# Kernel tuning notes

Hardware: AMD Instinct MI355X
Metric: run time of the kernel (lower is better)

## Reference

```python
import jax, jax.numpy as jnp
import numpy as np
from jax import lax

C, H, O = 95, 128, 4
B, T = 256, 1000
EPS = 1e-5


def setup_inputs() -> dict:
    key = jax.random.key(0)
    ks = jax.random.split(key, 8)
    x = jax.random.normal(ks[0], (B, T, C), dtype=jnp.float32)
    # BatchNorm1d params (eval mode: running stats)
    gamma = jnp.ones((C,), jnp.float32)
    beta = jnp.zeros((C,), jnp.float32)
    running_mean = jnp.zeros((C,), jnp.float32)
    running_var = jnp.ones((C,), jnp.float32)
    # LSTM params, torch gate order (i, f, g, o), init U(-1/sqrt(H), 1/sqrt(H))
    s = 1.0 / np.sqrt(H)
    W_ih = jax.random.uniform(ks[1], (4 * H, C), jnp.float32, -s, s)
    W_hh = jax.random.uniform(ks[2], (4 * H, H), jnp.float32, -s, s)
    b_ih = jax.random.uniform(ks[3], (4 * H,), jnp.float32, -s, s)
    b_hh = jax.random.uniform(ks[4], (4 * H,), jnp.float32, -s, s)
    # Final linear
    sf = 1.0 / np.sqrt(H)
    fc_w = jax.random.uniform(ks[5], (O, H), jnp.float32, -sf, sf)
    fc_b = jax.random.uniform(ks[6], (O,), jnp.float32, -sf, sf)
    return {"x": x, "gamma": gamma, "beta": beta,
            "running_mean": running_mean, "running_var": running_var,
            "W_ih": W_ih, "W_hh": W_hh, "b_ih": b_ih, "b_hh": b_hh,
            "fc_w": fc_w, "fc_b": fc_b}


def reference(x, gamma, beta, running_mean, running_var,
              W_ih, W_hh, b_ih, b_hh, fc_w, fc_b):
    # BatchNorm1d over channel dim (last axis of [B,T,C]), eval semantics
    inv = gamma * lax.rsqrt(running_var + EPS)
    xn = (x - running_mean) * inv + beta  # [B,T,C]
    # Precompute input contribution to all gates for every timestep
    xW = jnp.einsum('btc,gc->btg', xn, W_ih) + (b_ih + b_hh)  # [B,T,4H]

    def step(carry, xw_t):
        h, c = carry  # [B,H] each
        gates = xw_t + h @ W_hh.T  # [B,4H]
        i, f, g, o = jnp.split(gates, 4, axis=-1)
        i = jax.nn.sigmoid(i)
        f = jax.nn.sigmoid(f)
        g = jnp.tanh(g)
        o = jax.nn.sigmoid(o)
        c = f * c + i * g
        h = o * jnp.tanh(c)
        return (h, c), None

    h0 = jnp.zeros((x.shape[0], H), x.dtype)
    c0 = jnp.zeros((x.shape[0], H), x.dtype)
    (h_T, _), _ = lax.scan(step, (h0, c0), jnp.swapaxes(xW, 0, 1))  # scan over time
    return h_T @ fc_w.T + fc_b  # [B,O]
```

## Files before the change

### kernel.cpp

```cpp
#include <hip/hip_runtime.h>
#include <cstdint>

constexpr int Cc = 95;
constexpr int Hh = 128;
constexpr int G  = 512;
constexpr int Bb = 256;
constexpr int Tt = 1000;
#define EPSBN 1e-5f

typedef _Float16 half8  __attribute__((ext_vector_type(8)));
typedef float floatx4 __attribute__((ext_vector_type(4)));
typedef float float4u __attribute__((ext_vector_type(4), aligned(4)));
typedef float float2u __attribute__((ext_vector_type(2), aligned(4)));

__device__ __forceinline__ unsigned pku(float a, float b) {
  return __builtin_bit_cast(unsigned, __builtin_amdgcn_cvt_pkrtz(a, b));
}
__device__ __forceinline__ float fsigm(float y) {
  y = fminf(30.f, fmaxf(-30.f, y));
  float e = __expf(-y);
  return __fdividef(1.f, 1.f + e);
}
__device__ __forceinline__ float ftanh2(float x) {
  float y = fminf(30.f, fmaxf(-30.f, 2.f * x));
  float e = __expf(y);
  return __fdividef(e - 1.f, e + 1.f);
}

__global__ __launch_bounds__(512)
void k0_prep(const float* __restrict__ gamma, const float* __restrict__ beta,
             const float* __restrict__ rmean, const float* __restrict__ rvar,
             const float* __restrict__ W_ih, const float* __restrict__ b_ih,
             const float* __restrict__ b_hh, float* __restrict__ biasp,
             _Float16* __restrict__ Wp) {
  __shared__ float scl[Cc], sft[Cc];
  const int t = threadIdx.x;
  if (t < Cc) {
    float s = gamma[t] * rsqrtf(rvar[t] + EPSBN);
    scl[t] = s;
    sft[t] = beta[t] - rmean[t] * s;
  }
  __syncthreads();
  float acc = b_ih[t] + b_hh[t];
  const float* wr = W_ih + (size_t)t * Cc;
  for (int c = 0; c < Cc; ++c) {
    float w = wr[c];
    acc = fmaf(sft[c], w, acc);
    Wp[t * 96 + c] = (_Float16)(w * scl[c]);
  }
  Wp[t * 96 + 95] = (_Float16)0.f;
  biasp[t] = acc;
}

template <int TC>
__global__ __launch_bounds__(512)
void k1_mfma(const float* __restrict__ x, const _Float16* __restrict__ Wp,
             const float* __restrict__ biasp, _Float16* __restrict__ xw,
             int t0) {
  const int tid = threadIdx.x;
  const int wave = tid >> 6, lane = tid & 63;
  const int wm = wave >> 2, wn = wave & 3;
  const int row0 = blockIdx.x * 64 + wm * 32;
  const int nb0 = wn * 128;
  const int l15 = lane & 15, lg = lane >> 4;

  uint4 afr[2][3];
#pragma unroll
  for (int mt = 0; mt < 2; ++mt) {
    int m = row0 + mt * 16 + l15;
    int b = m / TC, tl = m - b * TC;
    const float* xr = x + ((size_t)b * Tt + t0 + tl) * Cc;
#pragma unroll
    for (int kk = 0; kk < 3; ++kk) {
      int k = kk * 32 + lg * 8;
      float4u p0 = *reinterpret_cast<const float4u*>(xr + k);
      float e4, e5, e6, e7;
      if (k == 88) {
        float2u q = *reinterpret_cast<const float2u*>(xr + 92);
        e4 = q[0]; e5 = q[1]; e6 = xr[94]; e7 = 0.f;
      } else {
        float4u p1 = *reinterpret_cast<const float4u*>(xr + k + 4);
        e4 = p1[0]; e5 = p1[1]; e6 = p1[2]; e7 = p1[3];
      }
      afr[mt][kk] = make_uint4(pku(p0[0], p0[1]), pku(p0[2], p0[3]),
                               pku(e4, e5), pku(e6, e7));
    }
  }

  floatx4 acc[2][8] = {};
#pragma unroll
  for (int kk = 0; kk < 3; ++kk)
#pragma unroll
    for (int nt = 0; nt < 8; ++nt) {
      const _Float16* wrow = Wp + (size_t)(nb0 + nt * 16 + l15) * 96 + lg * 8;
      uint4 bfr = *reinterpret_cast<const uint4*>(wrow + kk * 32);
      half8 bv = __builtin_bit_cast(half8, bfr);
      acc[0][nt] = __builtin_amdgcn_mfma_f32_16x16x32_f16(
          __builtin_bit_cast(half8, afr[0][kk]), bv, acc[0][nt], 0, 0, 0);
      acc[1][nt] = __builtin_amdgcn_mfma_f32_16x16x32_f16(
          __builtin_bit_cast(half8, afr[1][kk]), bv, acc[1][nt], 0, 0, 0);
    }

#pragma unroll
  for (int nt = 0; nt < 8; ++nt) {
    int n = nb0 + nt * 16 + l15;
    float bias = biasp[n];
#pragma unroll
    for (int mt = 0; mt < 2; ++mt) {
      int rbase = row0 + mt * 16 + lg * 4;
#pragma unroll
      for (int r = 0; r < 4; ++r)
        xw[(size_t)(rbase + r) * G + n] = (_Float16)(acc[mt][nt][r] + bias);
    }
  }
}

template <int TC>
__global__ __launch_bounds__(256, 1)
void k2_lstm(const _Float16* __restrict__ xw, const float* __restrict__ W_hh,
             float* __restrict__ hstate, float* __restrict__ cstate,
             const float* __restrict__ fc_w, const float* __restrict__ fc_b,
             float* __restrict__ out, int t0) {
  __shared__ __align__(16) _Float16 h2[2][Hh];
  __shared__ float h32[Hh];

  const int b = blockIdx.x;
  const int tid = threadIdx.x;
  const int w = tid >> 6, lane = tid & 63;
  const int l15 = lane & 15, lg = lane >> 4;
  const int hh = l15 & 1, rr = (l15 >> 1) & 3;
  const int u = 32 * w + 16 * hh + 4 * lg + rr;
  const bool owner = (l15 < 8);

  uint4 afr[8][4];
#pragma unroll
  for (int q = 0; q < 4; ++q)
#pragma unroll
    for (int h2i = 0; h2i < 2; ++h2i) {
      const float* wr =
          W_hh + (size_t)(q * 128 + 32 * w + 16 * h2i + l15) * Hh + 8 * lg;
#pragma unroll
      for (int kc = 0; kc < 4; ++kc) {
        float4u p0 = *reinterpret_cast<const float4u*>(wr + 32 * kc);
        float4u p1 = *reinterpret_cast<const float4u*>(wr + 32 * kc + 4);
        afr[2 * q + h2i][kc] = make_uint4(pku(p0[0], p0[1]), pku(p0[2], p0[3]),
                                          pku(p1[0], p1[1]), pku(p1[2], p1[3]));
      }
    }

  float creg = 0.f, hreg = 0.f;
  if (t0 == 0) {
    if (owner) h2[0][u] = (_Float16)0.f;
  } else {
    creg = cstate[b * Hh + u];
    hreg = hstate[b * Hh + u];
    if (owner) h2[0][u] = (_Float16)hreg;
  }
  __syncthreads();

  const _Float16* xwb = xw + (size_t)b * TC * G + u;

  float pi[4], pf[4], pg[4], po[4];
#pragma unroll
  for (int i = 0; i < 4; ++i) {
    if (i < TC) {
      const _Float16* xp = xwb + (size_t)i * G;
      pi[i] = (float)xp[0 * 128]; pf[i] = (float)xp[1 * 128];
      pg[i] = (float)xp[2 * 128]; po[i] = (float)xp[3 * 128];
    } else {
      pi[i] = pf[i] = pg[i] = po[i] = 0.f;
    }
  }

#define K2_STEP(TL, SL)                                                        \
  {                                                                            \
    const int tl_ = (TL);                                                      \
    const int rb_ = tl_ & 1;                                                   \
    float ci = pi[SL], cf = pf[SL], cg = pg[SL], co = po[SL];                  \
    if (tl_ + 4 < TC) {                                                        \
      const _Float16* xp_ = xwb + (size_t)(tl_ + 4) * G;                       \
      pi[SL] = (float)xp_[0 * 128]; pf[SL] = (float)xp_[1 * 128];              \
      pg[SL] = (float)xp_[2 * 128]; po[SL] = (float)xp_[3 * 128];              \
    }                                                                          \
    uint4 bfr[4];                                                              \
    _Pragma("unroll") for (int kc = 0; kc < 4; ++kc)                           \
        bfr[kc] = *reinterpret_cast<const uint4*>(&h2[rb_][32 * kc + 8 * lg]); \
    floatx4 acc[8] = {};                                                       \
    _Pragma("unroll") for (int kc = 0; kc < 4; ++kc)                           \
        _Pragma("unroll") for (int t_ = 0; t_ < 8; ++t_)                       \
            acc[t_] = __builtin_amdgcn_mfma_f32_16x16x32_f16(                  \
                __builtin_bit_cast(half8, afr[t_][kc]),                        \
                __builtin_bit_cast(half8, bfr[kc]), acc[t_], 0, 0, 0);         \
    float gq[4];                                                               \
    _Pragma("unroll") for (int q_ = 0; q_ < 4; ++q_) {                         \
      float e0 = hh ? acc[2 * q_ + 1][0] : acc[2 * q_][0];                     \
      float e1 = hh ? acc[2 * q_ + 1][1] : acc[2 * q_][1];                     \
      float e2 = hh ? acc[2 * q_ + 1][2] : acc[2 * q_][2];                     \
      float e3 = hh ? acc[2 * q_ + 1][3] : acc[2 * q_][3];                     \
      float lo = (rr & 1) ? e1 : e0;                                           \
      float hi = (rr & 1) ? e3 : e2;                                           \
      gq[q_] = (rr & 2) ? hi : lo;                                             \
    }                                                                          \
    float i_ = fsigm(gq[0] + ci);                                              \
    float f_ = fsigm(gq[1] + cf);                                              \
    float g_ = ftanh2(gq[2] + cg);                                             \
    float o_ = fsigm(gq[3] + co);                                              \
    creg = fmaf(f_, creg, i_ * g_);                                            \
    hreg = o_ * ftanh2(creg);                                                  \
    if (owner) h2[rb_ ^ 1][u] = (_Float16)hreg;                                \
    asm volatile("s_waitcnt lgkmcnt(0)" ::: "memory");                         \
    __builtin_amdgcn_s_barrier();                                              \
    __builtin_amdgcn_sched_barrier(0);                                         \
  }

  int tl = 0;
  for (; tl + 4 <= TC; tl += 4) {
    K2_STEP(tl + 0, 0)
    K2_STEP(tl + 1, 1)
    K2_STEP(tl + 2, 2)
    K2_STEP(tl + 3, 3)
  }
  if constexpr ((TC & 3) >= 1) K2_STEP(TC & ~3, 0)
  if constexpr ((TC & 3) >= 2) K2_STEP((TC & ~3) + 1, 1)
  if constexpr ((TC & 3) >= 3) K2_STEP((TC & ~3) + 2, 2)
#undef K2_STEP

  if (owner) {
    hstate[b * Hh + u] = hreg;
    cstate[b * Hh + u] = creg;
    h32[u] = hreg;
  }
  __syncthreads();

  if (t0 + TC == Tt && tid < 4) {
    float s = fc_b[tid];
    for (int jj = 0; jj < Hh; ++jj) s = fmaf(h32[jj], fc_w[tid * Hh + jj], s);
    out[b * 4 + tid] = s;
  }
}

template <int TC>
static void run_chunks(const float* x, const float* gamma, const float* beta,
                       const float* rmean, const float* rvar,
                       const float* W_ih, const float* W_hh,
                       const float* b_ih, const float* b_hh,
                       const float* fc_w, const float* fc_b, float* out,
                       void* d_ws, hipStream_t stream) {
  char* ws = reinterpret_cast<char*>(d_ws);
  _Float16* xwp = reinterpret_cast<_Float16*>(ws);
  size_t off = (size_t)Bb * TC * G * 4;
  float* hst = reinterpret_cast<float*>(ws + off);  off += (size_t)Bb * Hh * 4;
  float* cst = reinterpret_cast<float*>(ws + off);  off += (size_t)Bb * Hh * 4;
  float* bia = reinterpret_cast<float*>(ws + off);  off += 512 * 4;
  off = (off + 15) & ~(size_t)15;
  _Float16* Wp = reinterpret_cast<_Float16*>(ws + off);

  k0_prep<<<dim3(1), dim3(512), 0, stream>>>(gamma, beta, rmean, rvar, W_ih,
                                             b_ih, b_hh, bia, Wp);
  for (int t0 = 0; t0 < Tt; t0 += TC) {
    k1_mfma<TC><<<dim3(Bb * TC / 64), dim3(512), 0, stream>>>(x, Wp, bia, xwp,
                                                              t0);
    k2_lstm<TC><<<dim3(Bb), dim3(256), 0, stream>>>(xwp, W_hh, hst, cst, fc_w,
                                                    fc_b, out, t0);
  }
}

extern "C" void kernel_launch(void* const* d_in, const int* in_sizes, int n_in,
                              void* d_out, int out_size, void* d_ws,
                              size_t ws_size, hipStream_t stream) {
  const float* x     = (const float*)d_in[0];
  const float* gamma = (const float*)d_in[1];
  const float* beta  = (const float*)d_in[2];
  const float* rmean = (const float*)d_in[3];
  const float* rvar  = (const float*)d_in[4];
  const float* W_ih  = (const float*)d_in[5];
  const float* W_hh  = (const float*)d_in[6];
  const float* b_ih  = (const float*)d_in[7];
  const float* b_hh  = (const float*)d_in[8];
  const float* fc_w  = (const float*)d_in[9];
  const float* fc_b  = (const float*)d_in[10];
  float* out = (float*)d_out;

  auto need = [](int tc) {
    return (size_t)Bb * tc * G * 4 + 2 * (size_t)Bb * Hh * 4 + 512 * 4 + 16 +
           (size_t)512 * 96 * 2;
  };

  if (ws_size >= need(250)) {
    run_chunks<250>(x, gamma, beta, rmean, rvar, W_ih, W_hh, b_ih, b_hh, fc_w,
                    fc_b, out, d_ws, stream);
  } else if (ws_size >= need(125)) {
    run_chunks<125>(x, gamma, beta, rmean, rvar, W_ih, W_hh, b_ih, b_hh, fc_w,
                    fc_b, out, d_ws, stream);
  } else if (ws_size >= need(50)) {
    run_chunks<50>(x, gamma, beta, rmean, rvar, W_ih, W_hh, b_ih, b_hh, fc_w,
                   fc_b, out, d_ws, stream);
  } else {
    run_chunks<10>(x, gamma, beta, rmean, rvar, W_ih, W_hh, b_ih, b_hh, fc_w,
                   fc_b, out, d_ws, stream);
  }
}
```

Before: 932.4 us.

## Split recurrent gate matvec between MFMA and VALU dot2 paths

Each LSTM step previously ran all four gate blocks of W_hh·h through MFMA. Now the i and f gates are computed on the vector ALU, with each thread doing a 128-wide fp16 dot2 product against its own W_hh row held in registers, and the partner gate is exchanged via a lane shuffle. Only the g and o gates stay on MFMA. The intent is to halve the serial MFMA chain per timestep and overlap it with VALU work. In exchange it adds 64 weight registers per thread and 16 LDS reads of h per step. Prefetched xw values are also kept in fp16 to save registers.

```diff
diff --git a/kernel.cpp b/kernel.cpp
--- a/kernel.cpp
+++ b/kernel.cpp
@@ -9,12 +9,26 @@
 #define EPSBN 1e-5f
 
 typedef _Float16 half8  __attribute__((ext_vector_type(8)));
+typedef _Float16 half2v __attribute__((ext_vector_type(2)));
 typedef float floatx4 __attribute__((ext_vector_type(4)));
 typedef float float4u __attribute__((ext_vector_type(4), aligned(4)));
 typedef float float2u __attribute__((ext_vector_type(2), aligned(4)));
 
 __device__ __forceinline__ unsigned pku(float a, float b) {
   return __builtin_bit_cast(unsigned, __builtin_amdgcn_cvt_pkrtz(a, b));
+}
+__device__ __forceinline__ half2v pkh(float a, float b) {
+  return __builtin_bit_cast(half2v, __builtin_amdgcn_cvt_pkrtz(a, b));
+}
+__device__ __forceinline__ half2v bch(unsigned x) {
+  return __builtin_bit_cast(half2v, x);
+}
+__device__ __forceinline__ float fdot2(half2v a, half2v b, float c) {
+#if __has_builtin(__builtin_amdgcn_fdot2)
+  return __builtin_amdgcn_fdot2(a, b, c, false);
+#else
+  return fmaf((float)a[0], (float)b[0], fmaf((float)a[1], (float)b[1], c));
+#endif
 }
 __device__ __forceinline__ float fsigm(float y) {
   y = fminf(30.f, fmaxf(-30.f, y));
@@ -132,19 +146,30 @@
   const int u = 32 * w + 16 * hh + 4 * lg + rr;
   const bool owner = (l15 < 8);
 
-  uint4 afr[8][4];
-#pragma unroll
-  for (int q = 0; q < 4; ++q)
+  half2v wd[64];
+  {
+    const int rowd = (owner ? 0 : Hh) + u;
+    const float2* wr0 = reinterpret_cast<const float2*>(W_hh + (size_t)rowd * Hh);
+#pragma unroll
+    for (int i = 0; i < 64; ++i) {
+      float2 t = wr0[i];
+      wd[i] = pkh(t.x, t.y);
+    }
+  }
+
+  uint4 afr[4][4];
+#pragma unroll
+  for (int q2 = 0; q2 < 2; ++q2)
 #pragma unroll
     for (int h2i = 0; h2i < 2; ++h2i) {
-      const float* wr =
-          W_hh + (size_t)(q * 128 + 32 * w + 16 * h2i + l15) * Hh + 8 * lg;
+      const float* wr = W_hh +
+          (size_t)((q2 + 2) * 128 + 32 * w + 16 * h2i + l15) * Hh + 8 * lg;
 #pragma unroll
       for (int kc = 0; kc < 4; ++kc) {
         float4u p0 = *reinterpret_cast<const float4u*>(wr + 32 * kc);
         float4u p1 = *reinterpret_cast<const float4u*>(wr + 32 * kc + 4);
-        afr[2 * q + h2i][kc] = make_uint4(pku(p0[0], p0[1]), pku(p0[2], p0[3]),
-                                          pku(p1[0], p1[1]), pku(p1[2], p1[3]));
+        afr[2 * q2 + h2i][kc] = make_uint4(pku(p0[0], p0[1]), pku(p0[2], p0[3]),
+                                           pku(p1[0], p1[1]), pku(p1[2], p1[3]));
       }
     }
 
@@ -160,15 +185,15 @@
 
   const _Float16* xwb = xw + (size_t)b * TC * G + u;
 
-  float pi[4], pf[4], pg[4], po[4];
+  _Float16 ri[4], rf[4], rg[4], ro[4];
 #pragma unroll
   for (int i = 0; i < 4; ++i) {
     if (i < TC) {
       const _Float16* xp = xwb + (size_t)i * G;
-      pi[i] = (float)xp[0 * 128]; pf[i] = (float)xp[1 * 128];
-      pg[i] = (float)xp[2 * 128]; po[i] = (float)xp[3 * 128];
+      ri[i] = xp[0 * 128]; rf[i] = xp[1 * 128];
+      rg[i] = xp[2 * 128]; ro[i] = xp[3 * 128];
     } else {
-      pi[i] = pf[i] = pg[i] = po[i] = 0.f;
+      ri[i] = rf[i] = rg[i] = ro[i] = (_Float16)0.f;
     }
   }
 
@@ -176,35 +201,53 @@
   {                                                                            \
     const int tl_ = (TL);                                                      \
     const int rb_ = tl_ & 1;                                                   \
-    float ci = pi[SL], cf = pf[SL], cg = pg[SL], co = po[SL];                  \
+    float ci = (float)ri[SL], cf = (float)rf[SL];                              \
+    float cg = (float)rg[SL], co = (float)ro[SL];                              \
     if (tl_ + 4 < TC) {                                                        \
       const _Float16* xp_ = xwb + (size_t)(tl_ + 4) * G;                       \
-      pi[SL] = (float)xp_[0 * 128]; pf[SL] = (float)xp_[1 * 128];              \
-      pg[SL] = (float)xp_[2 * 128]; po[SL] = (float)xp_[3 * 128];              \
+      ri[SL] = xp_[0 * 128]; rf[SL] = xp_[1 * 128];                            \
+      rg[SL] = xp_[2 * 128]; ro[SL] = xp_[3 * 128];                            \
     }                                                                          \
     uint4 bfr[4];                                                              \
     _Pragma("unroll") for (int kc = 0; kc < 4; ++kc)                           \
         bfr[kc] = *reinterpret_cast<const uint4*>(&h2[rb_][32 * kc + 8 * lg]); \
-    floatx4 acc[8] = {};                                                       \
+    const uint4* hp_ = reinterpret_cast<const uint4*>(&h2[rb_][0]);            \
+    float a0 = 0.f, a1 = 0.f, a2 = 0.f, a3 = 0.f;                              \
+    _Pragma("unroll") for (int kk = 0; kk < 16; ++kk) {                        \
+      uint4 hv = hp_[kk];                                                      \
+      a0 = fdot2(wd[4 * kk + 0], bch(hv.x), a0);                               \
+      a1 = fdot2(wd[4 * kk + 1], bch(hv.y), a1);                               \
+      a2 = fdot2(wd[4 * kk + 2], bch(hv.z), a2);                               \
+      a3 = fdot2(wd[4 * kk + 3], bch(hv.w), a3);                               \
+    }                                                                          \
+    floatx4 acc[4] = {};                                                       \
     _Pragma("unroll") for (int kc = 0; kc < 4; ++kc)                           \
-        _Pragma("unroll") for (int t_ = 0; t_ < 8; ++t_)                       \
+        _Pragma("unroll") for (int t_ = 0; t_ < 4; ++t_)                       \
             acc[t_] = __builtin_amdgcn_mfma_f32_16x16x32_f16(                  \
                 __builtin_bit_cast(half8, afr[t_][kc]),                        \
                 __builtin_bit_cast(half8, bfr[kc]), acc[t_], 0, 0, 0);         \
-    float gq[4];                                                               \
-    _Pragma("unroll") for (int q_ = 0; q_ < 4; ++q_) {                         \
-      float e0 = hh ? acc[2 * q_ + 1][0] : acc[2 * q_][0];                     \
-      float e1 = hh ? acc[2 * q_ + 1][1] : acc[2 * q_][1];                     \
-      float e2 = hh ? acc[2 * q_ + 1][2] : acc[2 * q_][2];                     \
-      float e3 = hh ? acc[2 * q_ + 1][3] : acc[2 * q_][3];                     \
-      float lo = (rr & 1) ? e1 : e0;                                           \
-      float hi = (rr & 1) ? e3 : e2;                                           \
-      gq[q_] = (rr & 2) ? hi : lo;                                             \
-    }                                                                          \
-    float i_ = fsigm(gq[0] + ci);                                              \
-    float f_ = fsigm(gq[1] + cf);                                              \
-    float g_ = ftanh2(gq[2] + cg);                                             \
-    float o_ = fsigm(gq[3] + co);                                              \
+    float mydot = (a0 + a1) + (a2 + a3);                                       \
+    float othd = __shfl_xor(mydot, 8);                                         \
+    float dot_i = owner ? mydot : othd;                                        \
+    float dot_f = owner ? othd : mydot;                                        \
+    float eg0 = hh ? acc[1][0] : acc[0][0];                                    \
+    float eg1 = hh ? acc[1][1] : acc[0][1];                                    \
+    float eg2 = hh ? acc[1][2] : acc[0][2];                                    \
+    float eg3 = hh ? acc[1][3] : acc[0][3];                                    \
+    float glo = (rr & 1) ? eg1 : eg0;                                          \
+    float ghi = (rr & 1) ? eg3 : eg2;                                          \
+    float gg_ = (rr & 2) ? ghi : glo;                                          \
+    float eo0 = hh ? acc[3][0] : acc[2][0];                                    \
+    float eo1 = hh ? acc[3][1] : acc[2][1];                                    \
+    float eo2 = hh ? acc[3][2] : acc[2][2];                                    \
+    float eo3 = hh ? acc[3][3] : acc[2][3];                                    \
+    float olo = (rr & 1) ? eo1 : eo0;                                          \
+    float ohi = (rr & 1) ? eo3 : eo2;                                          \
+    float go_ = (rr & 2) ? ohi : olo;                                          \
+    float i_ = fsigm(dot_i + ci);                                              \
+    float f_ = fsigm(dot_f + cf);                                              \
+    float g_ = ftanh2(gg_ + cg);                                               \
+    float o_ = fsigm(go_ + co);                                                \
     creg = fmaf(f_, creg, i_ * g_);                                            \
     hreg = o_ * ftanh2(creg);                                                  \
     if (owner) h2[rb_ ^ 1][u] = (_Float16)hreg;                                \
```

After: 1.058 ms. 1.13x slower.

## Process two batch rows per LSTM block with 8 waves splitting hidden units

Applied to the files above, without the earlier changes.

The recurrent kernel now runs 128 blocks of 512 threads, each handling two batch rows. Each wave owns 16 hidden units across all four gates, so it holds half the W_hh fragments and issues 4 MFMAs per k-chunk instead of 8. The MFMA B operand's column lanes are shared between the two batch rows. The prefetched input-gate values are also kept in fp16 registers instead of fp32 to reduce register pressure. In exchange, every step's barrier now synchronises 8 waves instead of 4, only half as many blocks are launched, and most B-operand columns are wasted.

```diff
diff --git a/kernel.cpp b/kernel.cpp
--- a/kernel.cpp
+++ b/kernel.cpp
@@ -116,59 +116,59 @@
 }
 
 template <int TC>
-__global__ __launch_bounds__(256, 1)
+__global__ __attribute__((amdgpu_flat_work_group_size(512, 512)))
 void k2_lstm(const _Float16* __restrict__ xw, const float* __restrict__ W_hh,
              float* __restrict__ hstate, float* __restrict__ cstate,
              const float* __restrict__ fc_w, const float* __restrict__ fc_b,
              float* __restrict__ out, int t0) {
-  __shared__ __align__(16) _Float16 h2[2][Hh];
-  __shared__ float h32[Hh];
-
-  const int b = blockIdx.x;
+  __shared__ __align__(16) _Float16 h2[2][2][Hh];
+  __shared__ float h32[2][Hh];
+
   const int tid = threadIdx.x;
-  const int w = tid >> 6, lane = tid & 63;
+  const int W = tid >> 6, lane = tid & 63;
   const int l15 = lane & 15, lg = lane >> 4;
-  const int hh = l15 & 1, rr = (l15 >> 1) & 3;
-  const int u = 32 * w + 16 * hh + 4 * lg + rr;
+  const int bb = l15 & 1;
+  const int rr = (l15 >> 1) & 3;
+  const int u = 16 * W + 4 * lg + rr;
+  const int b = blockIdx.x * 2 + bb;
   const bool owner = (l15 < 8);
 
-  uint4 afr[8][4];
-#pragma unroll
-  for (int q = 0; q < 4; ++q)
-#pragma unroll
-    for (int h2i = 0; h2i < 2; ++h2i) {
-      const float* wr =
-          W_hh + (size_t)(q * 128 + 32 * w + 16 * h2i + l15) * Hh + 8 * lg;
-#pragma unroll
-      for (int kc = 0; kc < 4; ++kc) {
-        float4u p0 = *reinterpret_cast<const float4u*>(wr + 32 * kc);
-        float4u p1 = *reinterpret_cast<const float4u*>(wr + 32 * kc + 4);
-        afr[2 * q + h2i][kc] = make_uint4(pku(p0[0], p0[1]), pku(p0[2], p0[3]),
-                                          pku(p1[0], p1[1]), pku(p1[2], p1[3]));
-      }
-    }
+  uint4 afr[4][4];
+#pragma unroll
+  for (int q = 0; q < 4; ++q) {
+    const float* wr = W_hh + (size_t)(q * 128 + 16 * W + l15) * Hh + 8 * lg;
+#pragma unroll
+    for (int kc = 0; kc < 4; ++kc) {
+      float4u p0 = *reinterpret_cast<const float4u*>(wr + 32 * kc);
+      float4u p1 = *reinterpret_cast<const float4u*>(wr + 32 * kc + 4);
+      afr[q][kc] = make_uint4(pku(p0[0], p0[1]), pku(p0[2], p0[3]),
+                              pku(p1[0], p1[1]), pku(p1[2], p1[3]));
+    }
+  }
 
   float creg = 0.f, hreg = 0.f;
   if (t0 == 0) {
-    if (owner) h2[0][u] = (_Float16)0.f;
+    if (owner && lg == 0) {
+    }
+    if (owner) h2[bb][0][u] = (_Float16)0.f;
   } else {
     creg = cstate[b * Hh + u];
     hreg = hstate[b * Hh + u];
-    if (owner) h2[0][u] = (_Float16)hreg;
+    if (owner) h2[bb][0][u] = (_Float16)hreg;
   }
   __syncthreads();
 
   const _Float16* xwb = xw + (size_t)b * TC * G + u;
 
-  float pi[4], pf[4], pg[4], po[4];
+  _Float16 ri[4], rf[4], rg[4], ro[4];
 #pragma unroll
   for (int i = 0; i < 4; ++i) {
     if (i < TC) {
       const _Float16* xp = xwb + (size_t)i * G;
-      pi[i] = (float)xp[0 * 128]; pf[i] = (float)xp[1 * 128];
-      pg[i] = (float)xp[2 * 128]; po[i] = (float)xp[3 * 128];
+      ri[i] = xp[0 * 128]; rf[i] = xp[1 * 128];
+      rg[i] = xp[2 * 128]; ro[i] = xp[3 * 128];
     } else {
-      pi[i] = pf[i] = pg[i] = po[i] = 0.f;
+      ri[i] = rf[i] = rg[i] = ro[i] = (_Float16)0.f;
     }
   }
 
@@ -176,29 +176,26 @@
   {                                                                            \
     const int tl_ = (TL);                                                      \
     const int rb_ = tl_ & 1;                                                   \
-    float ci = pi[SL], cf = pf[SL], cg = pg[SL], co = po[SL];                  \
+    float ci = (float)ri[SL], cf = (float)rf[SL];                              \
+    float cg = (float)rg[SL], co = (float)ro[SL];                              \
     if (tl_ + 4 < TC) {                                                        \
       const _Float16* xp_ = xwb + (size_t)(tl_ + 4) * G;                       \
-      pi[SL] = (float)xp_[0 * 128]; pf[SL] = (float)xp_[1 * 128];              \
-      pg[SL] = (float)xp_[2 * 128]; po[SL] = (float)xp_[3 * 128];              \
+      ri[SL] = xp_[0 * 128]; rf[SL] = xp_[1 * 128];                            \
+      rg[SL] = xp_[2 * 128]; ro[SL] = xp_[3 * 128];                            \
     }                                                                          \
     uint4 bfr[4];                                                              \
+    _Pragma("unroll") for (int kc = 0; kc < 4; ++kc) bfr[kc] =                 \
+        *reinterpret_cast<const uint4*>(&h2[bb][rb_][32 * kc + 8 * lg]);       \
+    floatx4 acc[4] = {};                                                       \
     _Pragma("unroll") for (int kc = 0; kc < 4; ++kc)                           \
-        bfr[kc] = *reinterpret_cast<const uint4*>(&h2[rb_][32 * kc + 8 * lg]); \
-    floatx4 acc[8] = {};                                                       \
-    _Pragma("unroll") for (int kc = 0; kc < 4; ++kc)                           \
-        _Pragma("unroll") for (int t_ = 0; t_ < 8; ++t_)                       \
-            acc[t_] = __builtin_amdgcn_mfma_f32_16x16x32_f16(                  \
-                __builtin_bit_cast(half8, afr[t_][kc]),                        \
-                __builtin_bit_cast(half8, bfr[kc]), acc[t_], 0, 0, 0);         \
+        _Pragma("unroll") for (int q_ = 0; q_ < 4; ++q_)                       \
+            acc[q_] = __builtin_amdgcn_mfma_f32_16x16x32_f16(                  \
+                __builtin_bit_cast(half8, afr[q_][kc]),                        \
+                __builtin_bit_cast(half8, bfr[kc]), acc[q_], 0, 0, 0);         \
     float gq[4];                                                               \
     _Pragma("unroll") for (int q_ = 0; q_ < 4; ++q_) {                         \
-      float e0 = hh ? acc[2 * q_ + 1][0] : acc[2 * q_][0];                     \
-      float e1 = hh ? acc[2 * q_ + 1][1] : acc[2 * q_][1];                     \
-      float e2 = hh ? acc[2 * q_ + 1][2] : acc[2 * q_][2];                     \
-      float e3 = hh ? acc[2 * q_ + 1][3] : acc[2 * q_][3];                     \
-      float lo = (rr & 1) ? e1 : e0;                                           \
-      float hi = (rr & 1) ? e3 : e2;                                           \
+      float lo = (rr & 1) ? acc[q_][1] : acc[q_][0];                           \
+      float hi = (rr & 1) ? acc[q_][3] : acc[q_][2];                           \
       gq[q_] = (rr & 2) ? hi : lo;                                             \
     }                                                                          \
     float i_ = fsigm(gq[0] + ci);                                              \
@@ -207,7 +204,7 @@
     float o_ = fsigm(gq[3] + co);                                              \
     creg = fmaf(f_, creg, i_ * g_);                                            \
     hreg = o_ * ftanh2(creg);                                                  \
-    if (owner) h2[rb_ ^ 1][u] = (_Float16)hreg;                                \
+    if (owner) h2[bb][rb_ ^ 1][u] = (_Float16)hreg;                            \
     asm volatile("s_waitcnt lgkmcnt(0)" ::: "memory");                         \
     __builtin_amdgcn_s_barrier();                                              \
     __builtin_amdgcn_sched_barrier(0);                                         \
@@ -228,14 +225,17 @@
   if (owner) {
     hstate[b * Hh + u] = hreg;
     cstate[b * Hh + u] = creg;
-    h32[u] = hreg;
+    h32[bb][u] = hreg;
   }
   __syncthreads();
 
-  if (t0 + TC == Tt && tid < 4) {
-    float s = fc_b[tid];
-    for (int jj = 0; jj < Hh; ++jj) s = fmaf(h32[jj], fc_w[tid * Hh + jj], s);
-    out[b * 4 + tid] = s;
+  if (t0 + TC == Tt && tid < 8) {
+    int s2 = tid >> 2, g = tid & 3;
+    int bo = blockIdx.x * 2 + s2;
+    float s = fc_b[g];
+    for (int jj = 0; jj < Hh; ++jj)
+      s = fmaf(h32[s2][jj], fc_w[g * Hh + jj], s);
+    out[bo * 4 + g] = s;
   }
 }
 
@@ -260,8 +260,8 @@
   for (int t0 = 0; t0 < Tt; t0 += TC) {
     k1_mfma<TC><<<dim3(Bb * TC / 64), dim3(512), 0, stream>>>(x, Wp, bia, xwp,
                                                               t0);
-    k2_lstm<TC><<<dim3(Bb), dim3(256), 0, stream>>>(xwp, W_hh, hst, cst, fc_w,
-                                                    fc_b, out, t0);
+    k2_lstm<TC><<<dim3(Bb / 2), dim3(512), 0, stream>>>(xwp, W_hh, hst, cst,
+                                                        fc_w, fc_b, out, t0);
   }
 }
 
```

Result: faster. 900.6 us (-3.4%).

## Fuse projection and LSTM kernels, overlapping next-chunk GEMM with recurrence

Applied to the files above, without the earlier changes.

Combines the input-projection GEMM and the LSTM recurrence into a single kernel in which the first 256 blocks run the recurrence on the current chunk and the remaining blocks compute the projection for the next chunk into a second buffer. This hides the projection work behind the serial recurrence and removes one launch per chunk. Prefetched gate inputs are held as fp16 to save registers. The risk is that GEMM blocks share CUs with the latency-critical recurrence blocks and slow them down.

```diff
diff --git a/kernel.cpp b/kernel.cpp
--- a/kernel.cpp
+++ b/kernel.cpp
@@ -53,79 +53,78 @@
 }
 
 template <int TC>
-__global__ __launch_bounds__(512)
-void k1_mfma(const float* __restrict__ x, const _Float16* __restrict__ Wp,
-             const float* __restrict__ biasp, _Float16* __restrict__ xw,
-             int t0) {
+__global__ __launch_bounds__(256, 1)
+void k12(const float* __restrict__ x, const _Float16* __restrict__ Wp,
+         const float* __restrict__ biasp, const float* __restrict__ W_hh,
+         const _Float16* __restrict__ xw_r, _Float16* __restrict__ xw_w,
+         float* __restrict__ hstate, float* __restrict__ cstate,
+         const float* __restrict__ fc_w, const float* __restrict__ fc_b,
+         float* __restrict__ out, int n_k2, int t0r, int t0g) {
   const int tid = threadIdx.x;
-  const int wave = tid >> 6, lane = tid & 63;
-  const int wm = wave >> 2, wn = wave & 3;
-  const int row0 = blockIdx.x * 64 + wm * 32;
-  const int nb0 = wn * 128;
-  const int l15 = lane & 15, lg = lane >> 4;
-
-  uint4 afr[2][3];
-#pragma unroll
-  for (int mt = 0; mt < 2; ++mt) {
-    int m = row0 + mt * 16 + l15;
-    int b = m / TC, tl = m - b * TC;
-    const float* xr = x + ((size_t)b * Tt + t0 + tl) * Cc;
-#pragma unroll
-    for (int kk = 0; kk < 3; ++kk) {
-      int k = kk * 32 + lg * 8;
-      float4u p0 = *reinterpret_cast<const float4u*>(xr + k);
-      float e4, e5, e6, e7;
-      if (k == 88) {
-        float2u q = *reinterpret_cast<const float2u*>(xr + 92);
-        e4 = q[0]; e5 = q[1]; e6 = xr[94]; e7 = 0.f;
-      } else {
-        float4u p1 = *reinterpret_cast<const float4u*>(xr + k + 4);
-        e4 = p1[0]; e5 = p1[1]; e6 = p1[2]; e7 = p1[3];
+
+  if ((int)blockIdx.x >= n_k2) {
+    const int blk = blockIdx.x - n_k2;
+    const int wave = tid >> 6, lane = tid & 63;
+    const int nb0 = wave * 128;
+    const int row0 = blk * 32;
+    const int l15 = lane & 15, lg = lane >> 4;
+
+    uint4 afr[2][3];
+#pragma unroll
+    for (int mt = 0; mt < 2; ++mt) {
+      int m = row0 + mt * 16 + l15;
+      int b = m / TC, tl = m - b * TC;
+      const float* xr = x + ((size_t)b * Tt + t0g + tl) * Cc;
+#pragma unroll
+      for (int kk = 0; kk < 3; ++kk) {
+        int k = kk * 32 + lg * 8;
+        float4u p0 = *reinterpret_cast<const float4u*>(xr + k);
+        float e4, e5, e6, e7;
+        if (k == 88) {
+          float2u q = *reinterpret_cast<const float2u*>(xr + 92);
+          e4 = q[0]; e5 = q[1]; e6 = xr[94]; e7 = 0.f;
+        } else {
+          float4u p1 = *reinterpret_cast<const float4u*>(xr + k + 4);
+          e4 = p1[0]; e5 = p1[1]; e6 = p1[2]; e7 = p1[3];
+        }
+        afr[mt][kk] = make_uint4(pku(p0[0], p0[1]), pku(p0[2], p0[3]),
+                                 pku(e4, e5), pku(e6, e7));
       }
-      afr[mt][kk] = make_uint4(pku(p0[0], p0[1]), pku(p0[2], p0[3]),
-                               pku(e4, e5), pku(e6, e7));
     }
-  }
-
-  floatx4 acc[2][8] = {};
-#pragma unroll
-  for (int kk = 0; kk < 3; ++kk)
+
+    floatx4 acc[2][8] = {};
+#pragma unroll
+    for (int kk = 0; kk < 3; ++kk)
+#pragma unroll
+      for (int nt = 0; nt < 8; ++nt) {
+        const _Float16* wrow = Wp + (size_t)(nb0 + nt * 16 + l15) * 96 + lg * 8;
+        uint4 bfr = *reinterpret_cast<const uint4*>(wrow + kk * 32);
+        half8 bv = __builtin_bit_cast(half8, bfr);
+        acc[0][nt] = __builtin_amdgcn_mfma_f32_16x16x32_f16(
+            __builtin_bit_cast(half8, afr[0][kk]), bv, acc[0][nt], 0, 0, 0);
+        acc[1][nt] = __builtin_amdgcn_mfma_f32_16x16x32_f16(
+            __builtin_bit_cast(half8, afr[1][kk]), bv, acc[1][nt], 0, 0, 0);
+      }
+
 #pragma unroll
     for (int nt = 0; nt < 8; ++nt) {
-      const _Float16* wrow = Wp + (size_t)(nb0 + nt * 16 + l15) * 96 + lg * 8;
-      uint4 bfr = *reinterpret_cast<const uint4*>(wrow + kk * 32);
-      half8 bv = __builtin_bit_cast(half8, bfr);
-      acc[0][nt] = __builtin_amdgcn_mfma_f32_16x16x32_f16(
-          __builtin_bit_cast(half8, afr[0][kk]), bv, acc[0][nt], 0, 0, 0);
-      acc[1][nt] = __builtin_amdgcn_mfma_f32_16x16x32_f16(
-          __builtin_bit_cast(half8, afr[1][kk]), bv, acc[1][nt], 0, 0, 0);
+      int n = nb0 + nt * 16 + l15;
+      float bias = biasp[n];
+#pragma unroll
+      for (int mt = 0; mt < 2; ++mt) {
+        int rbase = row0 + mt * 16 + lg * 4;
+#pragma unroll
+        for (int r = 0; r < 4; ++r)
+          xw_w[(size_t)(rbase + r) * G + n] = (_Float16)(acc[mt][nt][r] + bias);
+      }
     }
-
-#pragma unroll
-  for (int nt = 0; nt < 8; ++nt) {
-    int n = nb0 + nt * 16 + l15;
-    float bias = biasp[n];
-#pragma unroll
-    for (int mt = 0; mt < 2; ++mt) {
-      int rbase = row0 + mt * 16 + lg * 4;
-#pragma unroll
-      for (int r = 0; r < 4; ++r)
-        xw[(size_t)(rbase + r) * G + n] = (_Float16)(acc[mt][nt][r] + bias);
-    }
-  }
-}
-
-template <int TC>
-__global__ __launch_bounds__(256, 1)
-void k2_lstm(const _Float16* __restrict__ xw, const float* __restrict__ W_hh,
-             float* __restrict__ hstate, float* __restrict__ cstate,
-             const float* __restrict__ fc_w, const float* __restrict__ fc_b,
-             float* __restrict__ out, int t0) {
+    return;
+  }
+
   __shared__ __align__(16) _Float16 h2[2][Hh];
   __shared__ float h32[Hh];
 
   const int b = blockIdx.x;
-  const int tid = threadIdx.x;
   const int w = tid >> 6, lane = tid & 63;
   const int l15 = lane & 15, lg = lane >> 4;
   const int hh = l15 & 1, rr = (l15 >> 1) & 3;
@@ -149,7 +148,7 @@
     }
 
   float creg = 0.f, hreg = 0.f;
-  if (t0 == 0) {
+  if (t0r == 0) {
     if (owner) h2[0][u] = (_Float16)0.f;
   } else {
     creg = cstate[b * Hh + u];
@@ -158,17 +157,17 @@
   }
   __syncthreads();
 
-  const _Float16* xwb = xw + (size_t)b * TC * G + u;
-
-  float pi[4], pf[4], pg[4], po[4];
+  const _Float16* xwb = xw_r + (size_t)b * TC * G + u;
+
+  _Float16 ri[4], rf[4], rg[4], ro[4];
 #pragma unroll
   for (int i = 0; i < 4; ++i) {
     if (i < TC) {
       const _Float16* xp = xwb + (size_t)i * G;
-      pi[i] = (float)xp[0 * 128]; pf[i] = (float)xp[1 * 128];
-      pg[i] = (float)xp[2 * 128]; po[i] = (float)xp[3 * 128];
+      ri[i] = xp[0 * 128]; rf[i] = xp[1 * 128];
+      rg[i] = xp[2 * 128]; ro[i] = xp[3 * 128];
     } else {
-      pi[i] = pf[i] = pg[i] = po[i] = 0.f;
+      ri[i] = rf[i] = rg[i] = ro[i] = (_Float16)0.f;
     }
   }
 
@@ -176,11 +175,12 @@
   {                                                                            \
     const int tl_ = (TL);                                                      \
     const int rb_ = tl_ & 1;                                                   \
-    float ci = pi[SL], cf = pf[SL], cg = pg[SL], co = po[SL];                  \
+    float ci = (float)ri[SL], cf = (float)rf[SL];                              \
+    float cg = (float)rg[SL], co = (float)ro[SL];                              \
     if (tl_ + 4 < TC) {                                                        \
       const _Float16* xp_ = xwb + (size_t)(tl_ + 4) * G;                       \
-      pi[SL] = (float)xp_[0 * 128]; pf[SL] = (float)xp_[1 * 128];              \
-      pg[SL] = (float)xp_[2 * 128]; po[SL] = (float)xp_[3 * 128];              \
+      ri[SL] = xp_[0 * 128]; rf[SL] = xp_[1 * 128];                            \
+      rg[SL] = xp_[2 * 128]; ro[SL] = xp_[3 * 128];                            \
     }                                                                          \
     uint4 bfr[4];                                                              \
     _Pragma("unroll") for (int kc = 0; kc < 4; ++kc)                           \
@@ -232,7 +232,7 @@
   }
   __syncthreads();
 
-  if (t0 + TC == Tt && tid < 4) {
+  if (t0r + TC == Tt && tid < 4) {
     float s = fc_b[tid];
     for (int jj = 0; jj < Hh; ++jj) s = fmaf(h32[jj], fc_w[tid * Hh + jj], s);
     out[b * 4 + tid] = s;
@@ -240,28 +240,37 @@
 }
 
 template <int TC>
-static void run_chunks(const float* x, const float* gamma, const float* beta,
-                       const float* rmean, const float* rvar,
-                       const float* W_ih, const float* W_hh,
-                       const float* b_ih, const float* b_hh,
-                       const float* fc_w, const float* fc_b, float* out,
-                       void* d_ws, hipStream_t stream) {
+static void run_all(const float* x, const float* gamma, const float* beta,
+                    const float* rmean, const float* rvar, const float* W_ih,
+                    const float* W_hh, const float* b_ih, const float* b_hh,
+                    const float* fc_w, const float* fc_b, float* out,
+                    void* d_ws, hipStream_t stream) {
   char* ws = reinterpret_cast<char*>(d_ws);
-  _Float16* xwp = reinterpret_cast<_Float16*>(ws);
-  size_t off = (size_t)Bb * TC * G * 4;
+  const size_t SX = (size_t)Bb * TC * G * 2;
+  _Float16* xwA = reinterpret_cast<_Float16*>(ws);
+  _Float16* xwB = reinterpret_cast<_Float16*>(ws + SX);
+  size_t off = 2 * SX;
   float* hst = reinterpret_cast<float*>(ws + off);  off += (size_t)Bb * Hh * 4;
   float* cst = reinterpret_cast<float*>(ws + off);  off += (size_t)Bb * Hh * 4;
   float* bia = reinterpret_cast<float*>(ws + off);  off += 512 * 4;
   off = (off + 15) & ~(size_t)15;
   _Float16* Wp = reinterpret_cast<_Float16*>(ws + off);
 
+  constexpr int NCH = Tt / TC;
+  constexpr int NK1 = Bb * TC / 32;
+
   k0_prep<<<dim3(1), dim3(512), 0, stream>>>(gamma, beta, rmean, rvar, W_ih,
                                              b_ih, b_hh, bia, Wp);
-  for (int t0 = 0; t0 < Tt; t0 += TC) {
-    k1_mfma<TC><<<dim3(Bb * TC / 64), dim3(512), 0, stream>>>(x, Wp, bia, xwp,
-                                                              t0);
-    k2_lstm<TC><<<dim3(Bb), dim3(256), 0, stream>>>(xwp, W_hh, hst, cst, fc_w,
-                                                    fc_b, out, t0);
+  k12<TC><<<dim3(NK1), dim3(256), 0, stream>>>(
+      x, Wp, bia, W_hh, nullptr, xwA, hst, cst, fc_w, fc_b, out, 0, 0, 0);
+
+  _Float16* bufs[2] = {xwA, xwB};
+  for (int c = 0; c < NCH; ++c) {
+    const bool last = (c == NCH - 1);
+    int grid = 256 + (last ? 0 : NK1);
+    k12<TC><<<dim3(grid), dim3(256), 0, stream>>>(
+        x, Wp, bia, W_hh, bufs[c & 1], bufs[(c + 1) & 1], hst, cst, fc_w, fc_b,
+        out, 256, c * TC, (c + 1) * TC);
   }
 }
 
@@ -282,21 +291,21 @@
   float* out = (float*)d_out;
 
   auto need = [](int tc) {
-    return (size_t)Bb * tc * G * 4 + 2 * (size_t)Bb * Hh * 4 + 512 * 4 + 16 +
-           (size_t)512 * 96 * 2;
+    return 2 * (size_t)Bb * tc * G * 2 + 2 * (size_t)Bb * Hh * 4 + 512 * 4 +
+           16 + (size_t)512 * 96 * 2;
   };
 
   if (ws_size >= need(250)) {
-    run_chunks<250>(x, gamma, beta, rmean, rvar, W_ih, W_hh, b_ih, b_hh, fc_w,
-                    fc_b, out, d_ws, stream);
+    run_all<250>(x, gamma, beta, rmean, rvar, W_ih, W_hh, b_ih, b_hh, fc_w,
+                 fc_b, out, d_ws, stream);
   } else if (ws_size >= need(125)) {
-    run_chunks<125>(x, gamma, beta, rmean, rvar, W_ih, W_hh, b_ih, b_hh, fc_w,
-                    fc_b, out, d_ws, stream);
+    run_all<125>(x, gamma, beta, rmean, rvar, W_ih, W_hh, b_ih, b_hh, fc_w,
+                 fc_b, out, d_ws, stream);
   } else if (ws_size >= need(50)) {
-    run_chunks<50>(x, gamma, beta, rmean, rvar, W_ih, W_hh, b_ih, b_hh, fc_w,
-                   fc_b, out, d_ws, stream);
+    run_all<50>(x, gamma, beta, rmean, rvar, W_ih, W_hh, b_ih, b_hh, fc_w,
+                fc_b, out, d_ws, stream);
   } else {
-    run_chunks<10>(x, gamma, beta, rmean, rvar, W_ih, W_hh, b_ih, b_hh, fc_w,
-                   fc_b, out, d_ws, stream);
-  }
-}
+    run_all<10>(x, gamma, beta, rmean, rvar, W_ih, W_hh, b_ih, b_hh, fc_w,
+                fc_b, out, d_ws, stream);
+  }
+}
```

Measured after the change: 809.1 us. 13.2% less time.
